# Optimization experiments

Measured on AMD Instinct MI355X. Metric: run time of the kernel, lower is better.

## Reference

```python
import jax, jax.numpy as jnp
import numpy as np

EPS = 1e-8  # torch cosine_similarity eps
B, N, M = 8192, 128, 64


def setup_inputs() -> dict:
    key = jax.random.key(0)
    ks = jax.random.split(key, 9)
    memory = jax.random.normal(ks[0], (B, N, M), dtype=jnp.float32) * 0.1
    prev_w = jax.random.uniform(ks[1], (B, N), dtype=jnp.float32)
    prev_w = prev_w / prev_w.sum(axis=1, keepdims=True)  # valid attention weighting
    k = jax.random.normal(ks[2], (B, M), dtype=jnp.float32)
    beta = jax.random.uniform(ks[3], (B, 1), dtype=jnp.float32) * 5.0  # key strength > 0
    g = jax.random.uniform(ks[4], (B, 1), dtype=jnp.float32)           # gate in [0,1)
    s = jax.nn.softmax(jax.random.normal(ks[5], (3,), dtype=jnp.float32))  # shift kernel
    y = 1.0 + jax.random.uniform(ks[6], (B, 1), dtype=jnp.float32) * 2.0   # sharpen >= 1
    e = jax.random.uniform(ks[7], (B, M), dtype=jnp.float32)           # erase in [0,1)
    a = jax.random.normal(ks[8], (B, M), dtype=jnp.float32)            # add vector
    return {"memory": memory, "prev_w": prev_w, "k": k, "beta": beta,
            "g": g, "s": s, "y": y, "e": e, "a": a}


def reference(memory, prev_w, k, beta, g, s, y, e, a):
    # --- content addressing: cosine similarity + softmax(beta * sim) ---
    dot = jnp.einsum('bm,bnm->bn', k, memory)                       # (B,N)
    k_norm = jnp.maximum(jnp.linalg.norm(k, axis=-1, keepdims=True), EPS)  # (B,1)
    m_norm = jnp.maximum(jnp.linalg.norm(memory, axis=-1), EPS)     # (B,N)
    cos = dot / (k_norm * m_norm)
    wc = jax.nn.softmax(beta * cos, axis=1)
    # --- interpolation with previous weighting ---
    wg = g * wc + (1.0 - g) * prev_w
    # --- circular convolution shift (cross-correlation with len-3 kernel, pad=1) ---
    # wt[b,i] = s[0]*wg[b,i-1] + s[1]*wg[b,i] + s[2]*wg[b,i+1]  (indices mod N)
    wt = s[0] * jnp.roll(wg, 1, axis=1) + s[1] * wg + s[2] * jnp.roll(wg, -1, axis=1)
    # --- sharpen: power then renormalize ---
    wp = wt ** y
    w = wp / wp.sum(axis=1, keepdims=True)
    # --- read from (old) memory ---
    read = jnp.einsum('bn,bnm->bm', w, memory)
    # --- erase/add write via batched outer products ---
    mem_new = memory * (1.0 - w[:, :, None] * e[:, None, :]) + w[:, :, None] * a[:, None, :]
    return read, mem_new, w
```

## Files before the change

### kernel.cpp

```cpp
#include <hip/hip_runtime.h>
#include <math.h>

constexpr int Bn = 8192;
constexpr int Nn = 128;
constexpr int Mn = 64;
constexpr float kEPS = 1e-8f;

constexpr int ROWP4 = 17;

__global__ __launch_bounds__(256)
void ntm_step(const float* __restrict__ memory,
              const float* __restrict__ prev_w,
              const float* __restrict__ kvec,
              const float* __restrict__ beta,
              const float* __restrict__ gate,
              const float* __restrict__ shift,
              const float* __restrict__ gamma,
              const float* __restrict__ erase,
              const float* __restrict__ addv,
              float* __restrict__ out_read,
              float* __restrict__ out_mem,
              float* __restrict__ out_w)
{
  __shared__ float lm[Nn * ROWP4 * 4];
  __shared__ float lk[Mn];
  __shared__ float le[Mn];
  __shared__ float la[Mn];
  __shared__ float llog[Nn];
  __shared__ float lwg[Nn];
  __shared__ float lw[Nn];
  __shared__ float lpart[16 * Mn];

  const int b = blockIdx.x;
  const int t = threadIdx.x;

  const float4* gm4 = (const float4*)(memory + (size_t)b * (Nn * Mn));

  if (t < Mn) {
    lk[t] = kvec[b * Mn + t];
    le[t] = erase[b * Mn + t];
    la[t] = addv[b * Mn + t];
  }

  float4 stg[8];
  #pragma unroll
  for (int i = 0; i < 8; ++i) stg[i] = gm4[t + 256 * i];
  #pragma unroll
  for (int i = 0; i < 8; ++i) {
    const int f = t + 256 * i;
    ((float4*)lm)[(f >> 4) * ROWP4 + (f & 15)] = stg[i];
  }
  __syncthreads();

  {
    const int n = t >> 1;
    const int half = t & 1;
    const float4* r4 = ((const float4*)lm) + n * ROWP4 + half * 8;
    const float4* k4 = ((const float4*)lk) + half * 8;
    float dot = 0.f, sq = 0.f, ksq = 0.f;
    #pragma unroll
    for (int j = 0; j < 8; ++j) {
      const float4 v = r4[j];
      const float4 kk = k4[j];
      dot += v.x * kk.x + v.y * kk.y + v.z * kk.z + v.w * kk.w;
      sq  += v.x * v.x + v.y * v.y + v.z * v.z + v.w * v.w;
      ksq += kk.x * kk.x + kk.y * kk.y + kk.z * kk.z + kk.w * kk.w;
    }
    dot += __shfl_xor(dot, 1);
    sq  += __shfl_xor(sq, 1);
    ksq += __shfl_xor(ksq, 1);
    if (half == 0) {
      const float kn = fmaxf(sqrtf(ksq), kEPS);
      const float mn = fmaxf(sqrtf(sq), kEPS);
      llog[n] = beta[b] * (dot / (kn * mn));
    }
  }
  __syncthreads();

  if (t < 64) {
    const float v0 = llog[t], v1 = llog[t + 64];
    float mx = fmaxf(v0, v1);
    #pragma unroll
    for (int o = 1; o < 64; o <<= 1) mx = fmaxf(mx, __shfl_xor(mx, o));
    const float e0 = __expf(v0 - mx), e1 = __expf(v1 - mx);
    float sum = e0 + e1;
    #pragma unroll
    for (int o = 1; o < 64; o <<= 1) sum += __shfl_xor(sum, o);
    const float inv = 1.f / sum;
    const float gv = gate[b];
    lwg[t]      = gv * (e0 * inv) + (1.f - gv) * prev_w[b * Nn + t];
    lwg[t + 64] = gv * (e1 * inv) + (1.f - gv) * prev_w[b * Nn + t + 64];
  }
  __syncthreads();

  if (t < 64) {
    const float s0 = shift[0], s1 = shift[1], s2 = shift[2];
    const int n0 = t, n1 = t + 64;
    const float wt0 = s0 * lwg[(n0 - 1) & 127] + s1 * lwg[n0] + s2 * lwg[(n0 + 1) & 127];
    const float wt1 = s0 * lwg[(n1 - 1) & 127] + s1 * lwg[n1] + s2 * lwg[(n1 + 1) & 127];
    const float yv = gamma[b];
    const float wp0 = powf(wt0, yv);
    const float wp1 = powf(wt1, yv);
    float sum = wp0 + wp1;
    #pragma unroll
    for (int o = 1; o < 64; o <<= 1) sum += __shfl_xor(sum, o);
    const float inv = 1.f / sum;
    const float w0 = wp0 * inv, w1 = wp1 * inv;
    lw[n0] = w0;
    lw[n1] = w1;
    out_w[b * Nn + n0] = w0;
    out_w[b * Nn + n1] = w1;
  }
  __syncthreads();

  {
    const int c4 = t & 15;
    const int rbase = t >> 4;
    const float4 ev = ((const float4*)le)[c4];
    const float4 av = ((const float4*)la)[c4];
    float4* om4 = (float4*)(out_mem + (size_t)b * (Nn * Mn));
    float4 racc = make_float4(0.f, 0.f, 0.f, 0.f);
    #pragma unroll
    for (int i = 0; i < 8; ++i) {
      const int row = rbase + 16 * i;
      const float wv = lw[row];
      const float4 mv = ((const float4*)lm)[row * ROWP4 + c4];
      float4 o;
      o.x = mv.x * (1.f - wv * ev.x) + wv * av.x;
      o.y = mv.y * (1.f - wv * ev.y) + wv * av.y;
      o.z = mv.z * (1.f - wv * ev.z) + wv * av.z;
      o.w = mv.w * (1.f - wv * ev.w) + wv * av.w;
      om4[t + 256 * i] = o;
      racc.x += wv * mv.x;
      racc.y += wv * mv.y;
      racc.z += wv * mv.z;
      racc.w += wv * mv.w;
    }
    ((float4*)lpart)[rbase * 16 + c4] = racc;
  }
  __syncthreads();

  if (t < Mn) {
    float acc = 0.f;
    #pragma unroll
    for (int p = 0; p < 16; ++p) acc += lpart[p * Mn + t];
    out_read[b * Mn + t] = acc;
  }
}

extern "C" void kernel_launch(void* const* d_in, const int* in_sizes, int n_in,
                              void* d_out, int out_size, void* d_ws, size_t ws_size,
                              hipStream_t stream) {
  const float* memory = (const float*)d_in[0];
  const float* prev_w = (const float*)d_in[1];
  const float* k      = (const float*)d_in[2];
  const float* beta   = (const float*)d_in[3];
  const float* g      = (const float*)d_in[4];
  const float* s      = (const float*)d_in[5];
  const float* y      = (const float*)d_in[6];
  const float* e      = (const float*)d_in[7];
  const float* a      = (const float*)d_in[8];

  float* out = (float*)d_out;
  float* out_read = out;
  float* out_mem  = out + (size_t)Bn * Mn;
  float* out_w    = out + (size_t)Bn * Mn + (size_t)Bn * Nn * Mn;

  ntm_step<<<Bn, 256, 0, stream>>>(memory, prev_w, k, beta, g, s, y, e, a,
                                   out_read, out_mem, out_w);
}
```

Before: 461.3 us.

## Keep memory tile in registers and compute row norms via wave shuffles

```diff
diff --git a/kernel.cpp b/kernel.cpp
--- a/kernel.cpp
+++ b/kernel.cpp
@@ -6,9 +6,8 @@
 constexpr int Mn = 64;
 constexpr float kEPS = 1e-8f;
 
-constexpr int ROWP4 = 17;
 
-__global__ __launch_bounds__(256)
+__global__ __launch_bounds__(256, 4)
 void ntm_step(const float* __restrict__ memory,
               const float* __restrict__ prev_w,
               const float* __restrict__ kvec,
@@ -22,57 +21,50 @@
               float* __restrict__ out_mem,
               float* __restrict__ out_w)
 {
-  __shared__ float lm[Nn * ROWP4 * 4];
-  __shared__ float lk[Mn];
-  __shared__ float le[Mn];
-  __shared__ float la[Mn];
   __shared__ float llog[Nn];
-  __shared__ float lwg[Nn];
   __shared__ float lw[Nn];
   __shared__ float lpart[16 * Mn];
 
   const int b = blockIdx.x;
   const int t = threadIdx.x;
+  const int c4 = t & 15;
+  const int rbase = t >> 4;
 
   const float4* gm4 = (const float4*)(memory + (size_t)b * (Nn * Mn));
-
-  if (t < Mn) {
-    lk[t] = kvec[b * Mn + t];
-    le[t] = erase[b * Mn + t];
-    la[t] = addv[b * Mn + t];
-  }
 
   float4 stg[8];
   #pragma unroll
   for (int i = 0; i < 8; ++i) stg[i] = gm4[t + 256 * i];
-  #pragma unroll
-  for (int i = 0; i < 8; ++i) {
-    const int f = t + 256 * i;
-    ((float4*)lm)[(f >> 4) * ROWP4 + (f & 15)] = stg[i];
-  }
-  __syncthreads();
+  const float4 k4 = ((const float4*)(kvec  + (size_t)b * Mn))[c4];
+  const float4 ev = ((const float4*)(erase + (size_t)b * Mn))[c4];
+  const float4 av = ((const float4*)(addv  + (size_t)b * Mn))[c4];
 
   {
-    const int n = t >> 1;
-    const int half = t & 1;
-    const float4* r4 = ((const float4*)lm) + n * ROWP4 + half * 8;
-    const float4* k4 = ((const float4*)lk) + half * 8;
-    float dot = 0.f, sq = 0.f, ksq = 0.f;
+    float dotp[8], sqp[8];
+    float ksq = k4.x * k4.x + k4.y * k4.y + k4.z * k4.z + k4.w * k4.w;
     #pragma unroll
-    for (int j = 0; j < 8; ++j) {
-      const float4 v = r4[j];
-      const float4 kk = k4[j];
-      dot += v.x * kk.x + v.y * kk.y + v.z * kk.z + v.w * kk.w;
-      sq  += v.x * v.x + v.y * v.y + v.z * v.z + v.w * v.w;
-      ksq += kk.x * kk.x + kk.y * kk.y + kk.z * kk.z + kk.w * kk.w;
+    for (int i = 0; i < 8; ++i) {
+      const float4 v = stg[i];
+      dotp[i] = v.x * k4.x + v.y * k4.y + v.z * k4.z + v.w * k4.w;
+      sqp[i]  = v.x * v.x + v.y * v.y + v.z * v.z + v.w * v.w;
     }
-    dot += __shfl_xor(dot, 1);
-    sq  += __shfl_xor(sq, 1);
-    ksq += __shfl_xor(ksq, 1);
-    if (half == 0) {
+    #pragma unroll
+    for (int o = 1; o < 16; o <<= 1) {
+      ksq += __shfl_xor(ksq, o);
+      #pragma unroll
+      for (int i = 0; i < 8; ++i) {
+        dotp[i] += __shfl_xor(dotp[i], o);
+        sqp[i]  += __shfl_xor(sqp[i], o);
+      }
+    }
+    if (c4 == 0) {
       const float kn = fmaxf(sqrtf(ksq), kEPS);
-      const float mn = fmaxf(sqrtf(sq), kEPS);
-      llog[n] = beta[b] * (dot / (kn * mn));
+      const float bv = beta[b];
+      #pragma unroll
+      for (int i = 0; i < 8; ++i) {
+        const float mn = fmaxf(sqrtf(sqp[i]), kEPS);
+        llog[rbase + 16 * i] = bv * (dotp[i] / (kn * mn));
+      }
     }
   }
   __syncthreads();
@@ -88,43 +80,45 @@
     for (int o = 1; o < 64; o <<= 1) sum += __shfl_xor(sum, o);
     const float inv = 1.f / sum;
     const float gv = gate[b];
-    lwg[t]      = gv * (e0 * inv) + (1.f - gv) * prev_w[b * Nn + t];
-    lwg[t + 64] = gv * (e1 * inv) + (1.f - gv) * prev_w[b * Nn + t + 64];
-  }
-  __syncthreads();
+    const float wg0 = gv * (e0 * inv) + (1.f - gv) * prev_w[b * Nn + t];
+    const float wg1 = gv * (e1 * inv) + (1.f - gv) * prev_w[b * Nn + t + 64];
 
-  if (t < 64) {
+    const int lm1 = (t + 63) & 63;
+    const int lp1 = (t + 1) & 63;
+    const float a0 = __shfl(wg0, lm1), a1 = __shfl(wg1, lm1);
+    const float b0 = __shfl(wg0, lp1), b1 = __shfl(wg1, lp1);
+    const float wm0 = (t == 0)  ? a1 : a0;
+    const float wp0i = (t == 63) ? b1 : b0;
+    const float wm1 = (t == 0)  ? a0 : a1;
+    const float wp1i = (t == 63) ? b0 : b1;
+
     const float s0 = shift[0], s1 = shift[1], s2 = shift[2];
-    const int n0 = t, n1 = t + 64;
-    const float wt0 = s0 * lwg[(n0 - 1) & 127] + s1 * lwg[n0] + s2 * lwg[(n0 + 1) & 127];
-    const float wt1 = s0 * lwg[(n1 - 1) & 127] + s1 * lwg[n1] + s2 * lwg[(n1 + 1) & 127];
+    const float wt0 = s0 * wm0 + s1 * wg0 + s2 * wp0i;
+    const float wt1 = s0 * wm1 + s1 * wg1 + s2 * wp1i;
+
     const float yv = gamma[b];
     const float wp0 = powf(wt0, yv);
     const float wp1 = powf(wt1, yv);
-    float sum = wp0 + wp1;
+    float psum = wp0 + wp1;
     #pragma unroll
-    for (int o = 1; o < 64; o <<= 1) sum += __shfl_xor(sum, o);
-    const float inv = 1.f / sum;
-    const float w0 = wp0 * inv, w1 = wp1 * inv;
-    lw[n0] = w0;
-    lw[n1] = w1;
-    out_w[b * Nn + n0] = w0;
-    out_w[b * Nn + n1] = w1;
+    for (int o = 1; o < 64; o <<= 1) psum += __shfl_xor(psum, o);
+    const float pinv = 1.f / psum;
+    const float w0 = wp0 * pinv, w1 = wp1 * pinv;
+    lw[t]      = w0;
+    lw[t + 64] = w1;
+    out_w[b * Nn + t]      = w0;
+    out_w[b * Nn + t + 64] = w1;
   }
   __syncthreads();
 
   {
-    const int c4 = t & 15;
-    const int rbase = t >> 4;
-    const float4 ev = ((const float4*)le)[c4];
-    const float4 av = ((const float4*)la)[c4];
     float4* om4 = (float4*)(out_mem + (size_t)b * (Nn * Mn));
     float4 racc = make_float4(0.f, 0.f, 0.f, 0.f);
     #pragma unroll
     for (int i = 0; i < 8; ++i) {
       const int row = rbase + 16 * i;
       const float wv = lw[row];
-      const float4 mv = ((const float4*)lm)[row * ROWP4 + c4];
+      const float4 mv = stg[i];
       float4 o;
       o.x = mv.x * (1.f - wv * ev.x) + wv * av.x;
       o.y = mv.y * (1.f - wv * ev.y) + wv * av.y;
```

After: 461.3 us. Within noise of the previous version (-0.0%).
